# Kernel optimization log

Measured on AMD Instinct MI355X. Metric: run time of the kernel, lower is better.

The kernel has to match this reference:

```python
import jax, jax.numpy as jnp
import numpy as np

A, B_, C = 270.0, 108.0, 0.154  # f-I transfer params
DT, I_0, TAU, GAMMA = 0.001, 0.334, 0.06, 0.641


def current_to_frequency(I):
    act = A * I - B_
    # freq = act / (1 - exp(-c*act)), with limit 1/c at act == 0
    zero = act == 0
    act_safe = jnp.where(zero, 1.0, act)  # avoid 0/0 in the unselected branch
    denom = 1.0 - jnp.exp(-C * act_safe)
    return jnp.where(zero, 1.0 / C, act_safe / denom)


def setup_inputs() -> dict:
    key = jax.random.key(0)
    k1, k2 = jax.random.split(key)
    Bsz, T = 8192, 2000
    Js, Jt = 0.35, 0.28387
    inp = jax.random.normal(k1, (Bsz, T, 2), dtype=jnp.float32)
    h0 = jax.random.uniform(k2, (1, Bsz, 2), dtype=jnp.float32)
    J = jnp.array([[(Js + Jt) / 2, (Jt - Js) / 2],
                   [(Jt - Js) / 2, (Js + Jt) / 2]], dtype=jnp.float32)
    return {"input": inp, "h0": h0, "J": J, "steps_per_bin": 4}


def reference(input, h0, J, steps_per_bin):
    # input: [B, T, 2], h0: [1, B, 2], J: [2, 2]
    sub_dt = DT / steps_per_bin

    def sub_step(state, _):
        current = state @ J + I_0 + sub_step.inp  # placeholder, replaced below
        return state, None

    def bin_step(state, inp_t):  # inp_t: [B, 2]
        def sub(state, _):
            current = state @ J + I_0 + inp_t
            rate = current_to_frequency(current)
            state = state + sub_dt * (-state / TAU + GAMMA * (1.0 - state) * rate)
            return state, rate
        state, rates = jax.lax.scan(sub, state, None, length=steps_per_bin)
        return state, (state, rates[-1])

    final, (states, rates) = jax.lax.scan(bin_step, h0[0], jnp.swapaxes(input, 0, 1))
    states = jnp.swapaxes(states, 0, 1)  # [B, T, 2]
    rates = jnp.swapaxes(rates, 0, 1)    # [B, T, 2]
    return states, rates, final[None]     # final: [1, B, 2]
```

## Files before the change

### kernel.cpp

```cpp
#include <hip/hip_runtime.h>


#define AF    270.0f
#define BF    108.0f
#define CF    0.154f
#define DTF   0.001f
#define I0F   0.334f
#define TAUF  0.06f
#define GAMF  0.641f
#define LOG2EF 1.44269504088896340736f
#define LN2F   0.69314718055994530942f

#if __has_builtin(__builtin_amdgcn_exp2f)
#define EXP2F(x) __builtin_amdgcn_exp2f(x)
#else
#define EXP2F(x) exp2f(x)
#endif

#if __has_builtin(__builtin_amdgcn_rcpf)
#define RCPF(x) __builtin_amdgcn_rcpf(x)
#else
#define RCPF(x) (1.0f / (x))
#endif

struct Consts {
  float X00, X10, X01, X11;
  float P, Q;
  float K1;
  float K2C;
  float INVC;
};

__device__ __forceinline__ void substep(const Consts& c, float xq0, float xq1,
                                        float& s0, float& s1, float& r20, float& r21) {
  float x0 = fmaf(c.X00, s0, fmaf(c.X10, s1, xq0));
  float x1 = fmaf(c.X01, s0, fmaf(c.X11, s1, xq1));
  float e0 = EXP2F(x0);
  float e1 = EXP2F(x1);
  float d0 = 1.0f - e0;
  float d1 = 1.0f - e1;
  float t0 = x0 * RCPF(d0);
  float t1 = x1 * RCPF(d1);
  r20 = (__builtin_fabsf(x0) < 1e-5f) ? -LOG2EF : t0;
  r21 = (__builtin_fabsf(x1) < 1e-5f) ? -LOG2EF : t1;
  float u0 = fmaf(-s0, r20, r20);
  float u1 = fmaf(-s1, r21, r21);
  s0 = fmaf(c.K2C, u0, c.K1 * s0);
  s1 = fmaf(c.K2C, u1, c.K1 * s1);
}

template <int SPB>
__device__ __forceinline__ void bin(const Consts& c, int spb, float in0, float in1,
                                    float& s0, float& s1, float& rt0, float& rt1) {
  float xq0 = fmaf(c.P, in0, c.Q);
  float xq1 = fmaf(c.P, in1, c.Q);
  float r20 = -LOG2EF, r21 = -LOG2EF;
  if (SPB > 0) {
#pragma unroll
    for (int k = 0; k < SPB; ++k) substep(c, xq0, xq1, s0, s1, r20, r21);
  } else {
    for (int k = 0; k < spb; ++k) substep(c, xq0, xq1, s0, s1, r20, r21);
  }
  rt0 = c.INVC * r20;
  rt1 = c.INVC * r21;
}

template <int SPB>
__device__ __forceinline__ void run_loop(const Consts& c, int spb, int T,
                                         const float* __restrict__ ip,
                                         float* __restrict__ sp, float* __restrict__ rp,
                                         float& s0, float& s1) {
  const int nch = T / 8;
  const float4* ip4 = (const float4*)ip;
  float4* sp4 = (float4*)sp;
  float4* rp4 = (float4*)rp;
  float4 bufA[4], bufB[4];
  if (nch > 0) {
#pragma unroll
    for (int i = 0; i < 4; ++i) { bufA[i] = ip4[i]; bufB[i] = bufA[i]; }
  }
  for (int ch = 0; ch < nch; ++ch) {
    if (ch + 1 < nch) {
#pragma unroll
      for (int i = 0; i < 4; ++i) bufB[i] = ip4[(ch + 1) * 4 + i];
    }
#pragma unroll
    for (int p = 0; p < 4; ++p) {
      float4 v = bufA[p];
      float rt0a, rt1a, rt0b, rt1b;
      bin<SPB>(c, spb, v.x, v.y, s0, s1, rt0a, rt1a);
      float s0a = s0, s1a = s1;
      bin<SPB>(c, spb, v.z, v.w, s0, s1, rt0b, rt1b);
      float4 st; st.x = s0a; st.y = s1a; st.z = s0; st.w = s1;
      float4 rt; rt.x = rt0a; rt.y = rt1a; rt.z = rt0b; rt.w = rt1b;
      sp4[ch * 4 + p] = st;
      rp4[ch * 4 + p] = rt;
    }
#pragma unroll
    for (int i = 0; i < 4; ++i) bufA[i] = bufB[i];
  }
  for (int t = nch * 8; t < T; ++t) {
    float in0 = ip[2 * t], in1 = ip[2 * t + 1];
    float rt0, rt1;
    bin<SPB>(c, spb, in0, in1, s0, s1, rt0, rt1);
    sp[2 * t] = s0; sp[2 * t + 1] = s1;
    rp[2 * t] = rt0; rp[2 * t + 1] = rt1;
  }
}

__global__ __launch_bounds__(64, 1)
void murray_kernel(const float* __restrict__ inp, const float* __restrict__ h0,
                   const float* __restrict__ Jm, const int* __restrict__ spb_p,
                   float* __restrict__ out, int B, int T) {
  const int b = blockIdx.x * 64 + threadIdx.x;
  if (b >= B) return;
  const int spb = *spb_p;

  const float J00 = Jm[0], J01 = Jm[1], J10 = Jm[2], J11 = Jm[3];
  const float sub_dt = DTF / (float)spb;
  const float NC = -CF * LOG2EF;

  Consts c;
  c.X00 = NC * AF * J00; c.X10 = NC * AF * J10;
  c.X01 = NC * AF * J01; c.X11 = NC * AF * J11;
  c.P   = NC * AF;
  c.Q   = NC * fmaf(AF, I0F, -BF);
  c.K1  = 1.0f - sub_dt / TAUF;
  c.INVC = -LN2F / CF;
  c.K2C = sub_dt * GAMF * c.INVC;

  float s0 = h0[2 * b], s1 = h0[2 * b + 1];

  const size_t row = (size_t)(2 * T);
  const float* ip = inp + (size_t)b * row;
  float* sp = out + (size_t)b * row;
  float* rp = out + (size_t)B * row + (size_t)b * row;
  float* fp = out + (size_t)B * row * 2 + (size_t)b * 2;

  if (spb == 4) {
    run_loop<4>(c, spb, T, ip, sp, rp, s0, s1);
  } else {
    run_loop<0>(c, spb, T, ip, sp, rp, s0, s1);
  }

  fp[0] = s0;
  fp[1] = s1;
}

extern "C" void kernel_launch(void* const* d_in, const int* in_sizes, int n_in,
                              void* d_out, int out_size, void* d_ws, size_t ws_size,
                              hipStream_t stream) {
  const float* inp = (const float*)d_in[0];
  const float* h0  = (const float*)d_in[1];
  const float* J   = (const float*)d_in[2];
  const int* spb   = (const int*)d_in[3];
  float* out = (float*)d_out;

  const int B = in_sizes[1] / 2;
  const int T = in_sizes[0] / (2 * B);
  const int blocks = (B + 63) / 64;

  murray_kernel<<<blocks, 64, 0, stream>>>(inp, h0, J, spb, out, B, T);
}
```

Measured before the change: 740.0 us.

## Split each batch row's two state components across lane pairs using DPP exchange

Each batch element now gets two threads, one per state component, which doubles the thread count. Partner states are exchanged every substep with a DPP quad swap. This halves the serial exp/rcp chain per thread and raises wave count, which helps latency hiding with only 128 waves originally. In exchange the loads and stores become scalar with stride 2 instead of float4 vectorized, a cross-lane dependency is added each substep, and the input prefetch is reworked into a rotating 8-deep buffer.

After: 659.8 us. 10.8% less time.

```diff
diff --git a/kernel.cpp b/kernel.cpp
--- a/kernel.cpp
+++ b/kernel.cpp
@@ -23,88 +23,74 @@
 #define RCPF(x) (1.0f / (x))
 #endif
 
+__device__ __forceinline__ float dpp_swap1(float v) {
+  return __int_as_float(
+      __builtin_amdgcn_mov_dpp(__float_as_int(v), 0xB1, 0xF, 0xF, true));
+}
+
 struct Consts {
-  float X00, X10, X01, X11;
+  float Xs, Xo;
   float P, Q;
   float K1;
   float K2C;
   float INVC;
 };
 
-__device__ __forceinline__ void substep(const Consts& c, float xq0, float xq1,
-                                        float& s0, float& s1, float& r20, float& r21) {
-  float x0 = fmaf(c.X00, s0, fmaf(c.X10, s1, xq0));
-  float x1 = fmaf(c.X01, s0, fmaf(c.X11, s1, xq1));
-  float e0 = EXP2F(x0);
-  float e1 = EXP2F(x1);
-  float d0 = 1.0f - e0;
-  float d1 = 1.0f - e1;
-  float t0 = x0 * RCPF(d0);
-  float t1 = x1 * RCPF(d1);
-  r20 = (__builtin_fabsf(x0) < 1e-5f) ? -LOG2EF : t0;
-  r21 = (__builtin_fabsf(x1) < 1e-5f) ? -LOG2EF : t1;
-  float u0 = fmaf(-s0, r20, r20);
-  float u1 = fmaf(-s1, r21, r21);
-  s0 = fmaf(c.K2C, u0, c.K1 * s0);
-  s1 = fmaf(c.K2C, u1, c.K1 * s1);
+__device__ __forceinline__ void substep(const Consts& c, float xq,
+                                        float& s, float& r2) {
+  float so = dpp_swap1(s);
+  float p  = fmaf(c.Xs, s, xq);
+  float x  = fmaf(c.Xo, so, p);
+  float e  = EXP2F(x);
+  float d  = 1.0f - e;
+  float t  = x * RCPF(d);
+  r2 = (__builtin_fabsf(x) < 1e-5f) ? -LOG2EF : t;
+  float u = fmaf(-s, r2, r2);
+  s = fmaf(c.K2C, u, c.K1 * s);
 }
 
 template <int SPB>
-__device__ __forceinline__ void bin(const Consts& c, int spb, float in0, float in1,
-                                    float& s0, float& s1, float& rt0, float& rt1) {
-  float xq0 = fmaf(c.P, in0, c.Q);
-  float xq1 = fmaf(c.P, in1, c.Q);
-  float r20 = -LOG2EF, r21 = -LOG2EF;
+__device__ __forceinline__ void bin(const Consts& c, int spb, float in,
+                                    float& s, float& rt) {
+  float xq = fmaf(c.P, in, c.Q);
+  float r2 = -LOG2EF;
   if (SPB > 0) {
 #pragma unroll
-    for (int k = 0; k < SPB; ++k) substep(c, xq0, xq1, s0, s1, r20, r21);
+    for (int k = 0; k < SPB; ++k) substep(c, xq, s, r2);
   } else {
-    for (int k = 0; k < spb; ++k) substep(c, xq0, xq1, s0, s1, r20, r21);
+    for (int k = 0; k < spb; ++k) substep(c, xq, s, r2);
   }
-  rt0 = c.INVC * r20;
-  rt1 = c.INVC * r21;
+  rt = c.INVC * r2;
 }
 
 template <int SPB>
 __device__ __forceinline__ void run_loop(const Consts& c, int spb, int T,
                                          const float* __restrict__ ip,
-                                         float* __restrict__ sp, float* __restrict__ rp,
-                                         float& s0, float& s1) {
-  const int nch = T / 8;
-  const float4* ip4 = (const float4*)ip;
-  float4* sp4 = (float4*)sp;
-  float4* rp4 = (float4*)rp;
-  float4 bufA[4], bufB[4];
-  if (nch > 0) {
+                                         float* __restrict__ sp,
+                                         float* __restrict__ rp, float& s) {
+  constexpr int PF = 8;
+  const int Tm1 = T - 1;
+  float buf[PF];
 #pragma unroll
-    for (int i = 0; i < 4; ++i) { bufA[i] = ip4[i]; bufB[i] = bufA[i]; }
+  for (int i = 0; i < PF; ++i) buf[i] = ip[2 * min(i, Tm1)];
+  int t0 = 0;
+  for (; t0 + PF <= T; t0 += PF) {
+#pragma unroll
+    for (int j = 0; j < PF; ++j) {
+      float nxt = ip[2 * min(t0 + PF + j, Tm1)];
+      float rt;
+      bin<SPB>(c, spb, buf[j], s, rt);
+      const int t = t0 + j;
+      sp[2 * t] = s;
+      rp[2 * t] = rt;
+      buf[j] = nxt;
+    }
   }
-  for (int ch = 0; ch < nch; ++ch) {
-    if (ch + 1 < nch) {
-#pragma unroll
-      for (int i = 0; i < 4; ++i) bufB[i] = ip4[(ch + 1) * 4 + i];
-    }
-#pragma unroll
-    for (int p = 0; p < 4; ++p) {
-      float4 v = bufA[p];
-      float rt0a, rt1a, rt0b, rt1b;
-      bin<SPB>(c, spb, v.x, v.y, s0, s1, rt0a, rt1a);
-      float s0a = s0, s1a = s1;
-      bin<SPB>(c, spb, v.z, v.w, s0, s1, rt0b, rt1b);
-      float4 st; st.x = s0a; st.y = s1a; st.z = s0; st.w = s1;
-      float4 rt; rt.x = rt0a; rt.y = rt1a; rt.z = rt0b; rt.w = rt1b;
-      sp4[ch * 4 + p] = st;
-      rp4[ch * 4 + p] = rt;
-    }
-#pragma unroll
-    for (int i = 0; i < 4; ++i) bufA[i] = bufB[i];
-  }
-  for (int t = nch * 8; t < T; ++t) {
-    float in0 = ip[2 * t], in1 = ip[2 * t + 1];
-    float rt0, rt1;
-    bin<SPB>(c, spb, in0, in1, s0, s1, rt0, rt1);
-    sp[2 * t] = s0; sp[2 * t + 1] = s1;
-    rp[2 * t] = rt0; rp[2 * t + 1] = rt1;
+  for (; t0 < T; ++t0) {
+    float rt;
+    bin<SPB>(c, spb, ip[2 * t0], s, rt);
+    sp[2 * t0] = s;
+    rp[2 * t0] = rt;
   }
 }
 
@@ -112,39 +98,41 @@
 void murray_kernel(const float* __restrict__ inp, const float* __restrict__ h0,
                    const float* __restrict__ Jm, const int* __restrict__ spb_p,
                    float* __restrict__ out, int B, int T) {
-  const int b = blockIdx.x * 64 + threadIdx.x;
-  if (b >= B) return;
+  const int tid = blockIdx.x * 64 + threadIdx.x;
+  const int cB = tid >> 1;
+  const int u  = tid & 1;
+  if (cB >= B) return;
   const int spb = *spb_p;
 
-  const float J00 = Jm[0], J01 = Jm[1], J10 = Jm[2], J11 = Jm[3];
+  const float Jself = u ? Jm[3] : Jm[0];
+  const float Joth  = u ? Jm[1] : Jm[2];
   const float sub_dt = DTF / (float)spb;
   const float NC = -CF * LOG2EF;
 
   Consts c;
-  c.X00 = NC * AF * J00; c.X10 = NC * AF * J10;
-  c.X01 = NC * AF * J01; c.X11 = NC * AF * J11;
-  c.P   = NC * AF;
-  c.Q   = NC * fmaf(AF, I0F, -BF);
-  c.K1  = 1.0f - sub_dt / TAUF;
+  c.Xs = NC * AF * Jself;
+  c.Xo = NC * AF * Joth;
+  c.P  = NC * AF;
+  c.Q  = NC * fmaf(AF, I0F, -BF);
+  c.K1 = 1.0f - sub_dt / TAUF;
   c.INVC = -LN2F / CF;
   c.K2C = sub_dt * GAMF * c.INVC;
 
-  float s0 = h0[2 * b], s1 = h0[2 * b + 1];
+  float s = h0[2 * cB + u];
 
   const size_t row = (size_t)(2 * T);
-  const float* ip = inp + (size_t)b * row;
-  float* sp = out + (size_t)b * row;
-  float* rp = out + (size_t)B * row + (size_t)b * row;
-  float* fp = out + (size_t)B * row * 2 + (size_t)b * 2;
+  const float* ip = inp + (size_t)cB * row + u;
+  float* sp = out + (size_t)cB * row + u;
+  float* rp = out + (size_t)B * row + (size_t)cB * row + u;
+  float* fp = out + (size_t)B * row * 2 + (size_t)(2 * cB + u);
 
   if (spb == 4) {
-    run_loop<4>(c, spb, T, ip, sp, rp, s0, s1);
+    run_loop<4>(c, spb, T, ip, sp, rp, s);
   } else {
-    run_loop<0>(c, spb, T, ip, sp, rp, s0, s1);
+    run_loop<0>(c, spb, T, ip, sp, rp, s);
   }
 
-  fp[0] = s0;
-  fp[1] = s1;
+  fp[0] = s;
 }
 
 extern "C" void kernel_launch(void* const* d_in, const int* in_sizes, int n_in,
@@ -158,7 +146,8 @@
 
   const int B = in_sizes[1] / 2;
   const int T = in_sizes[0] / (2 * B);
-  const int blocks = (B + 63) / 64;
+  const int threads = 2 * B;
+  const int blocks = (threads + 63) / 64;
 
   murray_kernel<<<blocks, 64, 0, stream>>>(inp, h0, J, spb, out, B, T);
 }
```
